# Performance work log

Measured on AMD Instinct MI355X. Metric: run time of the kernel, lower is better.

Reference implementation:

```python
import jax, jax.numpy as jnp
import numpy as np

N_NODES = 100000


def _add_self_loops(edge_index, n):
    loop = jnp.arange(n, dtype=edge_index.dtype)
    src = jnp.concatenate([edge_index[0], loop])
    dst = jnp.concatenate([edge_index[1], loop])
    return src, dst


def _gcn_conv(x, W, b, src, dst, n):
    # h = X W, then symmetric-normalized scatter-add over edges (PyG GCNConv)
    h = x @ W
    ones = jnp.ones(src.shape[0], dtype=h.dtype)
    deg = jax.ops.segment_sum(ones, dst, num_segments=n)  # in-degree incl. self loops
    dinv = jnp.where(deg > 0, jax.lax.rsqrt(deg), 0.0)
    norm = dinv[src] * dinv[dst]                           # [E]
    msg = h[src] * norm[:, None]                           # gather + scale
    out = jax.ops.segment_sum(msg, dst, num_segments=n)    # scatter-add
    return out + b


def setup_inputs() -> dict:
    key = jax.random.key(0)
    k1, k2, k3, k4 = jax.random.split(key, 4)
    F, H, C = 128, 128, 16
    x = jax.random.normal(k1, (N_NODES, F), dtype=jnp.float32)
    edge_index = jax.random.randint(k2, (2, 1600000), 0, N_NODES, dtype=jnp.int64)
    W1 = jax.random.normal(k3, (F, H), dtype=jnp.float32) / np.sqrt(F)
    b1 = jnp.zeros((H,), dtype=jnp.float32)
    W2 = jax.random.normal(k4, (H, C), dtype=jnp.float32) / np.sqrt(H)
    b2 = jnp.zeros((C,), dtype=jnp.float32)
    return {"x": x, "edge_index": edge_index, "W1": W1, "b1": b1, "W2": W2, "b2": b2}


def reference(x, edge_index, W1, b1, W2, b2):
    n = x.shape[0]
    src, dst = _add_self_loops(edge_index, n)
    h = _gcn_conv(x, W1, b1, src, dst, n)
    h = jax.nn.relu(h)
    # dropout(p=0.1) treated as identity (deterministic eval-mode reference)
    logits = _gcn_conv(h, W2, b2, src, dst, n)
    return logits, jax.nn.log_softmax(logits, axis=1)
```

## Files before the change

### kernel.cpp

```cpp
#include <hip/hip_runtime.h>
#include <math.h>


#define ELLW 72
#define EPB 16384
#define BSH 9
#define MAXBK 200
#define BCAP 10240

typedef __attribute__((ext_vector_type(8))) short short8;
typedef __attribute__((ext_vector_type(4))) float f32x4;
typedef __attribute__((ext_vector_type(4))) int i32x4;
typedef __attribute__((ext_vector_type(4))) _Float16 f16x4;
typedef __attribute__((ext_vector_type(8))) _Float16 f16x8;

__device__ __forceinline__ float bf2f(unsigned short u) {
    return __uint_as_float(((unsigned int)u) << 16);
}
__device__ __forceinline__ unsigned short f2bf(float f) {
    unsigned int u = __float_as_uint(f);
    unsigned int r = (u + 0x7fffu + ((u >> 16) & 1u)) >> 16;
    return (unsigned short)r;
}

__global__ __launch_bounds__(256) void k_bin_gemm(
        const int* __restrict__ src, const int* __restrict__ dst, int E,
        int* __restrict__ gcursor, int* __restrict__ binned, int nbuck, int neb,
        const float* __restrict__ x, const float* __restrict__ W1,
        unsigned short* __restrict__ h, int n) {
    __shared__ unsigned short xs[64 * 136];
    __shared__ unsigned short wtl[128 * 136];
    const int t = threadIdx.x;
    if ((int)blockIdx.x < neb) {
        int* cnt = (int*)xs;
        const int blk = blockIdx.x;
        for (int i = t; i < nbuck; i += 256) cnt[i] = 0;
        __syncthreads();
        const int e0 = blk * EPB;
        const int e1 = min(e0 + EPB, E);
        for (int e = e0 + t; e < e1; e += 256)
            atomicAdd(&cnt[dst[e] >> BSH], 1);
        __syncthreads();
        if (t < nbuck) {
            int c = cnt[t];
            cnt[t] = c ? atomicAdd(&gcursor[t], c) : 0;
        }
        __syncthreads();
        for (int e = e0 + t; e < e1; e += 256) {
            int d = dst[e];
            int b = d >> BSH;
            int r = atomicAdd(&cnt[b], 1);
            if (r < BCAP)
                binned[(size_t)b * BCAP + r] = src[e] | ((d & ((1 << BSH) - 1)) << 17);
        }
        return;
    }
    const int row0 = ((int)blockIdx.x - neb) * 64;
    for (int i = t; i < 2048; i += 256) {
        int r = i >> 5, c4 = (i & 31) << 2;
        int gr = row0 + r;
        float4 v = make_float4(0.f, 0.f, 0.f, 0.f);
        if (gr < n) v = *(const float4*)(x + (size_t)gr * 128 + c4);
        ushort4 u;
        u.x = f2bf(v.x); u.y = f2bf(v.y); u.z = f2bf(v.z); u.w = f2bf(v.w);
        *(ushort4*)(xs + r * 136 + c4) = u;
    }
    for (int i = t; i < 16384; i += 256) {
        int k = i >> 7, nc = i & 127;
        wtl[nc * 136 + k] = f2bf(W1[i]);
    }
    __syncthreads();
    const int w = t >> 6;
    const int lane = t & 63;
    const int m = lane & 15, q = lane >> 4;
    f32x4 acc[8];
#pragma unroll
    for (int ns = 0; ns < 8; ++ns) acc[ns] = (f32x4){0.f, 0.f, 0.f, 0.f};
#pragma unroll
    for (int kt = 0; kt < 4; ++kt) {
        short8 a = *(const short8*)(xs + (w * 16 + m) * 136 + kt * 32 + q * 8);
#pragma unroll
        for (int ns = 0; ns < 8; ++ns) {
            short8 b = *(const short8*)(wtl + (ns * 16 + m) * 136 + kt * 32 + q * 8);
            acc[ns] = __builtin_amdgcn_mfma_f32_16x16x32_bf16(a, b, acc[ns], 0, 0, 0);
        }
    }
    __syncthreads();
    unsigned short* xsw = xs + (w * 16) * 136;
#pragma unroll
    for (int ns = 0; ns < 8; ++ns)
#pragma unroll
        for (int reg = 0; reg < 4; ++reg)
            xsw[(q * 4 + reg) * 136 + ns * 16 + m] = f2bf(acc[ns][reg]);
    __syncthreads();
#pragma unroll
    for (int it = 0; it < 8; ++it) {
        int rl = (lane >> 5) + it * 2;
        int off = (lane & 31) * 4;
        int gr = row0 + w * 16 + rl;
        if (gr < n)
            *(ushort4*)(h + (size_t)gr * 128 + off) = *(const ushort4*)(xsw + rl * 136 + off);
    }
}

__global__ __launch_bounds__(256) void k_ell(
        const int* __restrict__ binned, const int* __restrict__ gcursor,
        int* __restrict__ deg, float* __restrict__ dinv, int* __restrict__ col,
        unsigned short* __restrict__ h, _Float16* __restrict__ g, int n) {
    __shared__ int sorted[BCAP];
    __shared__ int ldeg[1 << BSH];
    __shared__ int off[1 << BSH];
    __shared__ int cur[1 << BSH];
    __shared__ int psum[256];
    const int t = threadIdx.x, b = blockIdx.x;
    const int node0 = b << BSH;
    const size_t st = (size_t)b * BCAP;
    int cv = gcursor[b];
    if (cv > BCAP) cv = BCAP;
    if (b == 0) {
        if (t < 128) h[(size_t)n * 128 + t] = 0;
        if (t < 16) g[(size_t)n * 16 + t] = (_Float16)0.f;
        if (t == 0) dinv[n] = 1.f;
    }
    for (int i = t; i < (1 << BSH); i += 256) { ldeg[i] = 0; cur[i] = 0; }
    __syncthreads();
    for (int i = t; i < cv; i += 256)
        atomicAdd(&ldeg[binned[st + i] >> 17], 1);
    __syncthreads();
    int c0 = min(ldeg[2 * t], ELLW);
    int c1 = min(ldeg[2 * t + 1], ELLW);
    psum[t] = c0 + c1;
    __syncthreads();
    for (int o = 1; o < 256; o <<= 1) {
        int v = 0;
        if (t >= o) v = psum[t - o];
        __syncthreads();
        psum[t] += v;
        __syncthreads();
    }
    int base = psum[t] - (c0 + c1);
    off[2 * t] = base;
    off[2 * t + 1] = base + c0;
    __syncthreads();
    for (int i = t; i < cv; i += 256) {
        int v = binned[st + i];
        int dl = v >> 17;
        int r = atomicAdd(&cur[dl], 1);
        if (r < ELLW) sorted[off[dl] + r] = v & 0x1FFFF;
    }
    __syncthreads();
    const int nn = min(1 << BSH, n - node0);
    const int totv = nn * (ELLW / 4);
    int* colb = col + (size_t)node0 * ELLW;
    for (int idx = t; idx < totv; idx += 256) {
        int i = idx / (ELLW / 4);
        int q = (idx - i * (ELLW / 4)) * 4;
        int dc = min(ldeg[i], ELLW);
        int o = off[i];
        i32x4 v;
#pragma unroll
        for (int j = 0; j < 4; ++j)
            v[j] = (q + j < dc) ? sorted[o + q + j] : n;
        *(i32x4*)(colb + (size_t)i * ELLW + q) = v;
    }
    for (int i = t; i < (1 << BSH); i += 256) {
        int node = node0 + i;
        if (node < n) {
            int dgv = ldeg[i];
            deg[node] = dgv;
            dinv[node] = rsqrtf((float)(min(dgv, ELLW) + 1));
        }
    }
}

__global__ __launch_bounds__(256, 2) void k_gather1f(
        const unsigned short* __restrict__ h, const int* __restrict__ deg,
        const float* __restrict__ dinv, const int* __restrict__ col,
        const float* __restrict__ b1, const float* __restrict__ W2,
        _Float16* __restrict__ g, int n) {
    const int t = threadIdx.x;
    const int lane = t & 15;
    const int d = blockIdx.x * 16 + (t >> 4);
    if (d >= n) return;
    int dg = deg[d];
    if (dg > ELLW) dg = ELLW;
    const float dd = dinv[d];
    const int kend = (dg + 7) & ~7;
    const int* ecol = col + (size_t)d * ELLW;

    float aA[8], aB[8];
    {
        short8 u = *(const short8*)(h + (size_t)d * 128 + lane * 8);
#pragma unroll
        for (int j = 0; j < 8; ++j) {
            aA[j] = dd * bf2f((unsigned short)u[j]);
            aB[j] = 0.f;
        }
    }
    for (int k = 0; k < kend; k += 8) {
        int4 c0 = *(const int4*)(ecol + k);
        int4 c1 = *(const int4*)(ecol + k + 4);
        float e0 = dinv[c0.x], e1 = dinv[c0.y], e2 = dinv[c0.z], e3 = dinv[c0.w];
        float e4 = dinv[c1.x], e5 = dinv[c1.y], e6 = dinv[c1.z], e7 = dinv[c1.w];
        short8 u0 = *(const short8*)(h + (size_t)c0.x * 128 + lane * 8);
        short8 u1 = *(const short8*)(h + (size_t)c0.y * 128 + lane * 8);
        short8 u2 = *(const short8*)(h + (size_t)c0.z * 128 + lane * 8);
        short8 u3 = *(const short8*)(h + (size_t)c0.w * 128 + lane * 8);
        short8 u4 = *(const short8*)(h + (size_t)c1.x * 128 + lane * 8);
        short8 u5 = *(const short8*)(h + (size_t)c1.y * 128 + lane * 8);
        short8 u6 = *(const short8*)(h + (size_t)c1.z * 128 + lane * 8);
        short8 u7 = *(const short8*)(h + (size_t)c1.w * 128 + lane * 8);
#pragma unroll
        for (int j = 0; j < 8; ++j) {
            aA[j] = fmaf(bf2f((unsigned short)u0[j]), e0, aA[j]);
            aB[j] = fmaf(bf2f((unsigned short)u1[j]), e1, aB[j]);
            aA[j] = fmaf(bf2f((unsigned short)u2[j]), e2, aA[j]);
            aB[j] = fmaf(bf2f((unsigned short)u3[j]), e3, aB[j]);
            aA[j] = fmaf(bf2f((unsigned short)u4[j]), e4, aA[j]);
            aB[j] = fmaf(bf2f((unsigned short)u5[j]), e5, aB[j]);
            aA[j] = fmaf(bf2f((unsigned short)u6[j]), e6, aA[j]);
            aB[j] = fmaf(bf2f((unsigned short)u7[j]), e7, aB[j]);
        }
    }
    float y[8];
    const float* b1p = b1 + lane * 8;
#pragma unroll
    for (int j = 0; j < 8; ++j)
        y[j] = fmaxf(fmaf(aA[j] + aB[j], dd, b1p[j]), 0.f);
    const float4* w2v = (const float4*)(W2 + lane * 8 * 16);
    float4 z0 = make_float4(0.f, 0.f, 0.f, 0.f);
    float4 z1 = z0, z2 = z0, z3 = z0;
#pragma unroll
    for (int j = 0; j < 8; ++j) {
        float4 w0 = w2v[j * 4 + 0], w1 = w2v[j * 4 + 1];
        float4 w2 = w2v[j * 4 + 2], w3 = w2v[j * 4 + 3];
        float yj = y[j];
        z0.x = fmaf(yj, w0.x, z0.x); z0.y = fmaf(yj, w0.y, z0.y);
        z0.z = fmaf(yj, w0.z, z0.z); z0.w = fmaf(yj, w0.w, z0.w);
        z1.x = fmaf(yj, w1.x, z1.x); z1.y = fmaf(yj, w1.y, z1.y);
        z1.z = fmaf(yj, w1.z, z1.z); z1.w = fmaf(yj, w1.w, z1.w);
        z2.x = fmaf(yj, w2.x, z2.x); z2.y = fmaf(yj, w2.y, z2.y);
        z2.z = fmaf(yj, w2.z, z2.z); z2.w = fmaf(yj, w2.w, z2.w);
        z3.x = fmaf(yj, w3.x, z3.x); z3.y = fmaf(yj, w3.y, z3.y);
        z3.z = fmaf(yj, w3.z, z3.z); z3.w = fmaf(yj, w3.w, z3.w);
    }
#pragma unroll
    for (int mm = 1; mm < 16; mm <<= 1) {
        z0.x += __shfl_xor(z0.x, mm); z0.y += __shfl_xor(z0.y, mm);
        z0.z += __shfl_xor(z0.z, mm); z0.w += __shfl_xor(z0.w, mm);
        z1.x += __shfl_xor(z1.x, mm); z1.y += __shfl_xor(z1.y, mm);
        z1.z += __shfl_xor(z1.z, mm); z1.w += __shfl_xor(z1.w, mm);
        z2.x += __shfl_xor(z2.x, mm); z2.y += __shfl_xor(z2.y, mm);
        z2.z += __shfl_xor(z2.z, mm); z2.w += __shfl_xor(z2.w, mm);
        z3.x += __shfl_xor(z3.x, mm); z3.y += __shfl_xor(z3.y, mm);
        z3.z += __shfl_xor(z3.z, mm); z3.w += __shfl_xor(z3.w, mm);
    }
    if (lane < 4) {
        float4 z = (lane == 0) ? z0 : (lane == 1) ? z1 : (lane == 2) ? z2 : z3;
        f16x4 zz;
        zz[0] = (_Float16)(z.x * dd); zz[1] = (_Float16)(z.y * dd);
        zz[2] = (_Float16)(z.z * dd); zz[3] = (_Float16)(z.w * dd);
        *(f16x4*)(g + (size_t)d * 16 + lane * 4) = zz;
    }
}

__global__ void k_gather2(const _Float16* __restrict__ g, const int* __restrict__ deg,
                          const int* __restrict__ col, const float* __restrict__ b2,
                          float* __restrict__ out, int n) {
    const int t = threadIdx.x;
    const int d = blockIdx.x * 128 + (t >> 1);
    if (d >= n) return;
    const int l = t & 1;
    int dg = deg[d];
    if (dg > ELLW) dg = ELLW;
    const float dd = rsqrtf((float)(dg + 1));
    const int kend = (dg + 7) & ~7;
    const int* ecol = col + (size_t)d * ELLW;
    const _Float16* gl = g + l * 8;

    float aA[8], aB[8];
    {
        f16x8 s = *(const f16x8*)(gl + (size_t)d * 16);
#pragma unroll
        for (int j = 0; j < 8; ++j) { aA[j] = (float)s[j]; aB[j] = 0.f; }
    }
    for (int k = 0; k < kend; k += 8) {
        int4 c0 = *(const int4*)(ecol + k);
        int4 c1 = *(const int4*)(ecol + k + 4);
        f16x8 u0 = *(const f16x8*)(gl + (size_t)c0.x * 16);
        f16x8 u1 = *(const f16x8*)(gl + (size_t)c0.y * 16);
        f16x8 u2 = *(const f16x8*)(gl + (size_t)c0.z * 16);
        f16x8 u3 = *(const f16x8*)(gl + (size_t)c0.w * 16);
        f16x8 u4 = *(const f16x8*)(gl + (size_t)c1.x * 16);
        f16x8 u5 = *(const f16x8*)(gl + (size_t)c1.y * 16);
        f16x8 u6 = *(const f16x8*)(gl + (size_t)c1.z * 16);
        f16x8 u7 = *(const f16x8*)(gl + (size_t)c1.w * 16);
#pragma unroll
        for (int j = 0; j < 8; ++j) {
            aA[j] += (float)u0[j] + (float)u2[j] + (float)u4[j] + (float)u6[j];
            aB[j] += (float)u1[j] + (float)u3[j] + (float)u5[j] + (float)u7[j];
        }
    }
    float acc[8];
    const float* b2p = b2 + l * 8;
#pragma unroll
    for (int j = 0; j < 8; ++j) acc[j] = fmaf(aA[j] + aB[j], dd, b2p[j]);
    f32x4 o0 = {acc[0], acc[1], acc[2], acc[3]};
    f32x4 o1 = {acc[4], acc[5], acc[6], acc[7]};
    *(f32x4*)(out + (size_t)d * 16 + l * 8) = o0;
    *(f32x4*)(out + (size_t)d * 16 + l * 8 + 4) = o1;
    float m = acc[0];
#pragma unroll
    for (int j = 1; j < 8; ++j) m = fmaxf(m, acc[j]);
    m = fmaxf(m, __shfl_xor(m, 1));
    float e = 0.f;
#pragma unroll
    for (int j = 0; j < 8; ++j) e += expf(acc[j] - m);
    e += __shfl_xor(e, 1);
    float ls = m + logf(e);
    f32x4 p0, p1;
#pragma unroll
    for (int j = 0; j < 4; ++j) { p0[j] = acc[j] - ls; p1[j] = acc[j + 4] - ls; }
    float* ob = out + (size_t)n * 16 + (size_t)d * 16 + l * 8;
    *(f32x4*)(ob) = p0;
    *(f32x4*)(ob + 4) = p1;
}

static inline size_t align256(size_t v) { return (v + 255) & ~(size_t)255; }

extern "C" void kernel_launch(void* const* d_in, const int* in_sizes, int n_in,
                              void* d_out, int out_size, void* d_ws, size_t ws_size,
                              hipStream_t stream) {
    const float* x  = (const float*)d_in[0];
    const int*   ei = (const int*)d_in[1];
    const float* W1 = (const float*)d_in[2];
    const float* b1 = (const float*)d_in[3];
    const float* W2 = (const float*)d_in[4];
    const float* b2 = (const float*)d_in[5];
    float* out = (float*)d_out;

    const int n = in_sizes[0] / 128;
    const int E = in_sizes[1] / 2;
    const int* src = ei;
    const int* dst = ei + E;
    const int NEB = (E + EPB - 1) / EPB;
    const int NBUCK = (n + (1 << BSH) - 1) >> BSH;

    char* base = (char*)d_ws;
    size_t off = 0;
    int* deg = (int*)(base + off); off = align256(off + (size_t)n * 4);
    float* dinv = (float*)(base + off); off = align256(off + ((size_t)n + 1) * 4);
    int* col = (int*)(base + off); off = align256(off + (size_t)n * ELLW * 4);
    unsigned short* h = (unsigned short*)(base + off); off = align256(off + ((size_t)n + 1) * 128 * 2);
    _Float16* g = (_Float16*)(base + off); off = align256(off + ((size_t)n + 1) * 16 * 2);
    int* gcursor = (int*)(base + off); off = align256(off + (size_t)MAXBK * 4);
    int* binned = (int*)(base + off); off = align256(off + (size_t)NBUCK * BCAP * 4);

    hipMemsetAsync(gcursor, 0, (size_t)MAXBK * 4, stream);
    k_bin_gemm<<<NEB + (n + 63) / 64, 256, 0, stream>>>(
        src, dst, E, gcursor, binned, NBUCK, NEB, x, W1, h, n);
    k_ell<<<NBUCK, 256, 0, stream>>>(binned, gcursor, deg, dinv, col, h, g, n);
    k_gather1f<<<(n + 15) / 16, 256, 0, stream>>>(h, deg, dinv, col, b1, W2, g, n);
    k_gather2<<<(n + 127) / 128, 256, 0, stream>>>(g, deg, col, b2, out, n);
}
```

Baseline: 332.6 us.

## Fuse four GCN kernels into one persistent cooperative kernel with grid syncs

New measurement: 523.9 us. 1.58x slower.

```diff
diff --git a/kernel.cpp b/kernel.cpp
--- a/kernel.cpp
+++ b/kernel.cpp
@@ -1,5 +1,8 @@
 #include <hip/hip_runtime.h>
+#include <hip/hip_cooperative_groups.h>
 #include <math.h>
+
+namespace cg = cooperative_groups;
 
 
 #define ELLW 72
@@ -23,307 +26,318 @@
     return (unsigned short)r;
 }
 
-__global__ __launch_bounds__(256) void k_bin_gemm(
+__global__ __launch_bounds__(256) void k_fused(
         const int* __restrict__ src, const int* __restrict__ dst, int E,
         int* __restrict__ gcursor, int* __restrict__ binned, int nbuck, int neb,
         const float* __restrict__ x, const float* __restrict__ W1,
-        unsigned short* __restrict__ h, int n) {
-    __shared__ unsigned short xs[64 * 136];
-    __shared__ unsigned short wtl[128 * 136];
+        unsigned short* __restrict__ wt, unsigned short* __restrict__ h, int n,
+        int* __restrict__ deg, float* __restrict__ dinv, int* __restrict__ col,
+        const float* __restrict__ b1, const float* __restrict__ W2,
+        _Float16* __restrict__ g, const float* __restrict__ b2,
+        float* __restrict__ out, int gtiles, int t1, int t2) {
+    cg::grid_group grid = cg::this_grid();
+    __shared__ int smem_i[12032];
     const int t = threadIdx.x;
-    if ((int)blockIdx.x < neb) {
-        int* cnt = (int*)xs;
-        const int blk = blockIdx.x;
-        for (int i = t; i < nbuck; i += 256) cnt[i] = 0;
-        __syncthreads();
-        const int e0 = blk * EPB;
-        const int e1 = min(e0 + EPB, E);
-        for (int e = e0 + t; e < e1; e += 256)
-            atomicAdd(&cnt[dst[e] >> BSH], 1);
-        __syncthreads();
-        if (t < nbuck) {
-            int c = cnt[t];
-            cnt[t] = c ? atomicAdd(&gcursor[t], c) : 0;
-        }
-        __syncthreads();
-        for (int e = e0 + t; e < e1; e += 256) {
-            int d = dst[e];
-            int b = d >> BSH;
-            int r = atomicAdd(&cnt[b], 1);
-            if (r < BCAP)
-                binned[(size_t)b * BCAP + r] = src[e] | ((d & ((1 << BSH) - 1)) << 17);
-        }
-        return;
-    }
-    const int row0 = ((int)blockIdx.x - neb) * 64;
-    for (int i = t; i < 2048; i += 256) {
-        int r = i >> 5, c4 = (i & 31) << 2;
-        int gr = row0 + r;
-        float4 v = make_float4(0.f, 0.f, 0.f, 0.f);
-        if (gr < n) v = *(const float4*)(x + (size_t)gr * 128 + c4);
-        ushort4 u;
-        u.x = f2bf(v.x); u.y = f2bf(v.y); u.z = f2bf(v.z); u.w = f2bf(v.w);
-        *(ushort4*)(xs + r * 136 + c4) = u;
-    }
-    for (int i = t; i < 16384; i += 256) {
-        int k = i >> 7, nc = i & 127;
-        wtl[nc * 136 + k] = f2bf(W1[i]);
-    }
-    __syncthreads();
-    const int w = t >> 6;
-    const int lane = t & 63;
-    const int m = lane & 15, q = lane >> 4;
-    f32x4 acc[8];
-#pragma unroll
-    for (int ns = 0; ns < 8; ++ns) acc[ns] = (f32x4){0.f, 0.f, 0.f, 0.f};
-#pragma unroll
-    for (int kt = 0; kt < 4; ++kt) {
-        short8 a = *(const short8*)(xs + (w * 16 + m) * 136 + kt * 32 + q * 8);
-#pragma unroll
-        for (int ns = 0; ns < 8; ++ns) {
-            short8 b = *(const short8*)(wtl + (ns * 16 + m) * 136 + kt * 32 + q * 8);
-            acc[ns] = __builtin_amdgcn_mfma_f32_16x16x32_bf16(a, b, acc[ns], 0, 0, 0);
-        }
-    }
-    __syncthreads();
-    unsigned short* xsw = xs + (w * 16) * 136;
-#pragma unroll
-    for (int ns = 0; ns < 8; ++ns)
-#pragma unroll
-        for (int reg = 0; reg < 4; ++reg)
-            xsw[(q * 4 + reg) * 136 + ns * 16 + m] = f2bf(acc[ns][reg]);
-    __syncthreads();
-#pragma unroll
-    for (int it = 0; it < 8; ++it) {
-        int rl = (lane >> 5) + it * 2;
-        int off = (lane & 31) * 4;
-        int gr = row0 + w * 16 + rl;
-        if (gr < n)
-            *(ushort4*)(h + (size_t)gr * 128 + off) = *(const ushort4*)(xsw + rl * 136 + off);
-    }
-}
-
-__global__ __launch_bounds__(256) void k_ell(
-        const int* __restrict__ binned, const int* __restrict__ gcursor,
-        int* __restrict__ deg, float* __restrict__ dinv, int* __restrict__ col,
-        unsigned short* __restrict__ h, _Float16* __restrict__ g, int n) {
-    __shared__ int sorted[BCAP];
-    __shared__ int ldeg[1 << BSH];
-    __shared__ int off[1 << BSH];
-    __shared__ int cur[1 << BSH];
-    __shared__ int psum[256];
-    const int t = threadIdx.x, b = blockIdx.x;
-    const int node0 = b << BSH;
-    const size_t st = (size_t)b * BCAP;
-    int cv = gcursor[b];
-    if (cv > BCAP) cv = BCAP;
-    if (b == 0) {
+    const int nb = gridDim.x;
+
+    for (int i = blockIdx.x * 256 + t; i < 16384 + MAXBK; i += nb * 256) {
+        if (i < 16384) {
+            int nc = i >> 7, k = i & 127;
+            wt[i] = f2bf(W1[k * 128 + nc]);
+        } else {
+            gcursor[i - 16384] = 0;
+        }
+    }
+    if (blockIdx.x == 0) {
         if (t < 128) h[(size_t)n * 128 + t] = 0;
         if (t < 16) g[(size_t)n * 16 + t] = (_Float16)0.f;
         if (t == 0) dinv[n] = 1.f;
     }
-    for (int i = t; i < (1 << BSH); i += 256) { ldeg[i] = 0; cur[i] = 0; }
-    __syncthreads();
-    for (int i = t; i < cv; i += 256)
-        atomicAdd(&ldeg[binned[st + i] >> 17], 1);
-    __syncthreads();
-    int c0 = min(ldeg[2 * t], ELLW);
-    int c1 = min(ldeg[2 * t + 1], ELLW);
-    psum[t] = c0 + c1;
-    __syncthreads();
-    for (int o = 1; o < 256; o <<= 1) {
-        int v = 0;
-        if (t >= o) v = psum[t - o];
+    grid.sync();
+
+    for (int tile = blockIdx.x; tile < neb + gtiles; tile += nb) {
         __syncthreads();
-        psum[t] += v;
-        __syncthreads();
-    }
-    int base = psum[t] - (c0 + c1);
-    off[2 * t] = base;
-    off[2 * t + 1] = base + c0;
-    __syncthreads();
-    for (int i = t; i < cv; i += 256) {
-        int v = binned[st + i];
-        int dl = v >> 17;
-        int r = atomicAdd(&cur[dl], 1);
-        if (r < ELLW) sorted[off[dl] + r] = v & 0x1FFFF;
-    }
-    __syncthreads();
-    const int nn = min(1 << BSH, n - node0);
-    const int totv = nn * (ELLW / 4);
-    int* colb = col + (size_t)node0 * ELLW;
-    for (int idx = t; idx < totv; idx += 256) {
-        int i = idx / (ELLW / 4);
-        int q = (idx - i * (ELLW / 4)) * 4;
-        int dc = min(ldeg[i], ELLW);
-        int o = off[i];
-        i32x4 v;
-#pragma unroll
-        for (int j = 0; j < 4; ++j)
-            v[j] = (q + j < dc) ? sorted[o + q + j] : n;
-        *(i32x4*)(colb + (size_t)i * ELLW + q) = v;
-    }
-    for (int i = t; i < (1 << BSH); i += 256) {
-        int node = node0 + i;
-        if (node < n) {
-            int dgv = ldeg[i];
-            deg[node] = dgv;
-            dinv[node] = rsqrtf((float)(min(dgv, ELLW) + 1));
-        }
-    }
-}
-
-__global__ __launch_bounds__(256, 2) void k_gather1f(
-        const unsigned short* __restrict__ h, const int* __restrict__ deg,
-        const float* __restrict__ dinv, const int* __restrict__ col,
-        const float* __restrict__ b1, const float* __restrict__ W2,
-        _Float16* __restrict__ g, int n) {
-    const int t = threadIdx.x;
-    const int lane = t & 15;
-    const int d = blockIdx.x * 16 + (t >> 4);
-    if (d >= n) return;
-    int dg = deg[d];
-    if (dg > ELLW) dg = ELLW;
-    const float dd = dinv[d];
-    const int kend = (dg + 7) & ~7;
-    const int* ecol = col + (size_t)d * ELLW;
-
-    float aA[8], aB[8];
+        if (tile < neb) {
+            int* cnt = smem_i;
+            for (int i = t; i < nbuck; i += 256) cnt[i] = 0;
+            __syncthreads();
+            const int e0 = tile * EPB;
+            const int e1 = min(e0 + EPB, E);
+            for (int e = e0 + t; e < e1; e += 256)
+                atomicAdd(&cnt[dst[e] >> BSH], 1);
+            __syncthreads();
+            if (t < nbuck) {
+                int c = cnt[t];
+                cnt[t] = c ? atomicAdd(&gcursor[t], c) : 0;
+            }
+            __syncthreads();
+            for (int e = e0 + t; e < e1; e += 256) {
+                int d = dst[e];
+                int b = d >> BSH;
+                int r = atomicAdd(&cnt[b], 1);
+                if (r < BCAP)
+                    binned[(size_t)b * BCAP + r] =
+                        src[e] | ((d & ((1 << BSH) - 1)) << 17);
+            }
+        } else {
+            unsigned short* xs = (unsigned short*)smem_i;
+            const int row0 = (tile - neb) * 64;
+            for (int i = t; i < 2048; i += 256) {
+                int r = i >> 5, c4 = (i & 31) << 2;
+                int gr = row0 + r;
+                float4 v = make_float4(0.f, 0.f, 0.f, 0.f);
+                if (gr < n) v = *(const float4*)(x + (size_t)gr * 128 + c4);
+                ushort4 u;
+                u.x = f2bf(v.x); u.y = f2bf(v.y); u.z = f2bf(v.z); u.w = f2bf(v.w);
+                *(ushort4*)(xs + r * 136 + c4) = u;
+            }
+            __syncthreads();
+            const int w = t >> 6;
+            const int lane = t & 63;
+            const int m = lane & 15, q = lane >> 4;
+            f32x4 acc[8];
+#pragma unroll
+            for (int ns = 0; ns < 8; ++ns) acc[ns] = (f32x4){0.f, 0.f, 0.f, 0.f};
+#pragma unroll
+            for (int kt = 0; kt < 4; ++kt) {
+                short8 a = *(const short8*)(xs + (w * 16 + m) * 136 + kt * 32 + q * 8);
+#pragma unroll
+                for (int ns = 0; ns < 8; ++ns) {
+                    short8 b = *(const short8*)((const short*)wt +
+                               (ns * 16 + m) * 128 + kt * 32 + q * 8);
+                    acc[ns] = __builtin_amdgcn_mfma_f32_16x16x32_bf16(a, b, acc[ns], 0, 0, 0);
+                }
+            }
+            unsigned short* xsw = xs + (w * 16) * 136;
+#pragma unroll
+            for (int ns = 0; ns < 8; ++ns)
+#pragma unroll
+                for (int reg = 0; reg < 4; ++reg)
+                    xsw[(q * 4 + reg) * 136 + ns * 16 + m] = f2bf(acc[ns][reg]);
+            __syncthreads();
+#pragma unroll
+            for (int it = 0; it < 8; ++it) {
+                int rl = (lane >> 5) + it * 2;
+                int offb = (lane & 31) * 4;
+                int gr = row0 + w * 16 + rl;
+                if (gr < n)
+                    *(ushort4*)(h + (size_t)gr * 128 + offb) =
+                        *(const ushort4*)(xsw + rl * 136 + offb);
+            }
+        }
+    }
+    grid.sync();
+
     {
-        short8 u = *(const short8*)(h + (size_t)d * 128 + lane * 8);
-#pragma unroll
-        for (int j = 0; j < 8; ++j) {
-            aA[j] = dd * bf2f((unsigned short)u[j]);
-            aB[j] = 0.f;
-        }
-    }
-    for (int k = 0; k < kend; k += 8) {
-        int4 c0 = *(const int4*)(ecol + k);
-        int4 c1 = *(const int4*)(ecol + k + 4);
-        float e0 = dinv[c0.x], e1 = dinv[c0.y], e2 = dinv[c0.z], e3 = dinv[c0.w];
-        float e4 = dinv[c1.x], e5 = dinv[c1.y], e6 = dinv[c1.z], e7 = dinv[c1.w];
-        short8 u0 = *(const short8*)(h + (size_t)c0.x * 128 + lane * 8);
-        short8 u1 = *(const short8*)(h + (size_t)c0.y * 128 + lane * 8);
-        short8 u2 = *(const short8*)(h + (size_t)c0.z * 128 + lane * 8);
-        short8 u3 = *(const short8*)(h + (size_t)c0.w * 128 + lane * 8);
-        short8 u4 = *(const short8*)(h + (size_t)c1.x * 128 + lane * 8);
-        short8 u5 = *(const short8*)(h + (size_t)c1.y * 128 + lane * 8);
-        short8 u6 = *(const short8*)(h + (size_t)c1.z * 128 + lane * 8);
-        short8 u7 = *(const short8*)(h + (size_t)c1.w * 128 + lane * 8);
-#pragma unroll
-        for (int j = 0; j < 8; ++j) {
-            aA[j] = fmaf(bf2f((unsigned short)u0[j]), e0, aA[j]);
-            aB[j] = fmaf(bf2f((unsigned short)u1[j]), e1, aB[j]);
-            aA[j] = fmaf(bf2f((unsigned short)u2[j]), e2, aA[j]);
-            aB[j] = fmaf(bf2f((unsigned short)u3[j]), e3, aB[j]);
-            aA[j] = fmaf(bf2f((unsigned short)u4[j]), e4, aA[j]);
-            aB[j] = fmaf(bf2f((unsigned short)u5[j]), e5, aB[j]);
-            aA[j] = fmaf(bf2f((unsigned short)u6[j]), e6, aA[j]);
-            aB[j] = fmaf(bf2f((unsigned short)u7[j]), e7, aB[j]);
-        }
-    }
-    float y[8];
-    const float* b1p = b1 + lane * 8;
-#pragma unroll
-    for (int j = 0; j < 8; ++j)
-        y[j] = fmaxf(fmaf(aA[j] + aB[j], dd, b1p[j]), 0.f);
-    const float4* w2v = (const float4*)(W2 + lane * 8 * 16);
-    float4 z0 = make_float4(0.f, 0.f, 0.f, 0.f);
-    float4 z1 = z0, z2 = z0, z3 = z0;
-#pragma unroll
-    for (int j = 0; j < 8; ++j) {
-        float4 w0 = w2v[j * 4 + 0], w1 = w2v[j * 4 + 1];
-        float4 w2 = w2v[j * 4 + 2], w3 = w2v[j * 4 + 3];
-        float yj = y[j];
-        z0.x = fmaf(yj, w0.x, z0.x); z0.y = fmaf(yj, w0.y, z0.y);
-        z0.z = fmaf(yj, w0.z, z0.z); z0.w = fmaf(yj, w0.w, z0.w);
-        z1.x = fmaf(yj, w1.x, z1.x); z1.y = fmaf(yj, w1.y, z1.y);
-        z1.z = fmaf(yj, w1.z, z1.z); z1.w = fmaf(yj, w1.w, z1.w);
-        z2.x = fmaf(yj, w2.x, z2.x); z2.y = fmaf(yj, w2.y, z2.y);
-        z2.z = fmaf(yj, w2.z, z2.z); z2.w = fmaf(yj, w2.w, z2.w);
-        z3.x = fmaf(yj, w3.x, z3.x); z3.y = fmaf(yj, w3.y, z3.y);
-        z3.z = fmaf(yj, w3.z, z3.z); z3.w = fmaf(yj, w3.w, z3.w);
-    }
-#pragma unroll
-    for (int mm = 1; mm < 16; mm <<= 1) {
-        z0.x += __shfl_xor(z0.x, mm); z0.y += __shfl_xor(z0.y, mm);
-        z0.z += __shfl_xor(z0.z, mm); z0.w += __shfl_xor(z0.w, mm);
-        z1.x += __shfl_xor(z1.x, mm); z1.y += __shfl_xor(z1.y, mm);
-        z1.z += __shfl_xor(z1.z, mm); z1.w += __shfl_xor(z1.w, mm);
-        z2.x += __shfl_xor(z2.x, mm); z2.y += __shfl_xor(z2.y, mm);
-        z2.z += __shfl_xor(z2.z, mm); z2.w += __shfl_xor(z2.w, mm);
-        z3.x += __shfl_xor(z3.x, mm); z3.y += __shfl_xor(z3.y, mm);
-        z3.z += __shfl_xor(z3.z, mm); z3.w += __shfl_xor(z3.w, mm);
-    }
-    if (lane < 4) {
-        float4 z = (lane == 0) ? z0 : (lane == 1) ? z1 : (lane == 2) ? z2 : z3;
-        f16x4 zz;
-        zz[0] = (_Float16)(z.x * dd); zz[1] = (_Float16)(z.y * dd);
-        zz[2] = (_Float16)(z.z * dd); zz[3] = (_Float16)(z.w * dd);
-        *(f16x4*)(g + (size_t)d * 16 + lane * 4) = zz;
-    }
-}
-
-__global__ void k_gather2(const _Float16* __restrict__ g, const int* __restrict__ deg,
-                          const int* __restrict__ col, const float* __restrict__ b2,
-                          float* __restrict__ out, int n) {
-    const int t = threadIdx.x;
-    const int d = blockIdx.x * 128 + (t >> 1);
-    if (d >= n) return;
-    const int l = t & 1;
-    int dg = deg[d];
-    if (dg > ELLW) dg = ELLW;
-    const float dd = rsqrtf((float)(dg + 1));
-    const int kend = (dg + 7) & ~7;
-    const int* ecol = col + (size_t)d * ELLW;
-    const _Float16* gl = g + l * 8;
-
-    float aA[8], aB[8];
-    {
-        f16x8 s = *(const f16x8*)(gl + (size_t)d * 16);
-#pragma unroll
-        for (int j = 0; j < 8; ++j) { aA[j] = (float)s[j]; aB[j] = 0.f; }
-    }
-    for (int k = 0; k < kend; k += 8) {
-        int4 c0 = *(const int4*)(ecol + k);
-        int4 c1 = *(const int4*)(ecol + k + 4);
-        f16x8 u0 = *(const f16x8*)(gl + (size_t)c0.x * 16);
-        f16x8 u1 = *(const f16x8*)(gl + (size_t)c0.y * 16);
-        f16x8 u2 = *(const f16x8*)(gl + (size_t)c0.z * 16);
-        f16x8 u3 = *(const f16x8*)(gl + (size_t)c0.w * 16);
-        f16x8 u4 = *(const f16x8*)(gl + (size_t)c1.x * 16);
-        f16x8 u5 = *(const f16x8*)(gl + (size_t)c1.y * 16);
-        f16x8 u6 = *(const f16x8*)(gl + (size_t)c1.z * 16);
-        f16x8 u7 = *(const f16x8*)(gl + (size_t)c1.w * 16);
-#pragma unroll
-        for (int j = 0; j < 8; ++j) {
-            aA[j] += (float)u0[j] + (float)u2[j] + (float)u4[j] + (float)u6[j];
-            aB[j] += (float)u1[j] + (float)u3[j] + (float)u5[j] + (float)u7[j];
-        }
-    }
-    float acc[8];
-    const float* b2p = b2 + l * 8;
-#pragma unroll
-    for (int j = 0; j < 8; ++j) acc[j] = fmaf(aA[j] + aB[j], dd, b2p[j]);
-    f32x4 o0 = {acc[0], acc[1], acc[2], acc[3]};
-    f32x4 o1 = {acc[4], acc[5], acc[6], acc[7]};
-    *(f32x4*)(out + (size_t)d * 16 + l * 8) = o0;
-    *(f32x4*)(out + (size_t)d * 16 + l * 8 + 4) = o1;
-    float m = acc[0];
-#pragma unroll
-    for (int j = 1; j < 8; ++j) m = fmaxf(m, acc[j]);
-    m = fmaxf(m, __shfl_xor(m, 1));
-    float e = 0.f;
-#pragma unroll
-    for (int j = 0; j < 8; ++j) e += expf(acc[j] - m);
-    e += __shfl_xor(e, 1);
-    float ls = m + logf(e);
-    f32x4 p0, p1;
-#pragma unroll
-    for (int j = 0; j < 4; ++j) { p0[j] = acc[j] - ls; p1[j] = acc[j + 4] - ls; }
-    float* ob = out + (size_t)n * 16 + (size_t)d * 16 + l * 8;
-    *(f32x4*)(ob) = p0;
-    *(f32x4*)(ob + 4) = p1;
+        int* sorted = smem_i;
+        int* ldeg   = smem_i + BCAP;
+        int* offv   = smem_i + BCAP + 512;
+        int* cur    = smem_i + BCAP + 1024;
+        int* psum   = smem_i + BCAP + 1536;
+        for (int b = blockIdx.x; b < nbuck; b += nb) {
+            __syncthreads();
+            const int node0 = b << BSH;
+            const size_t st = (size_t)b * BCAP;
+            int cv = gcursor[b];
+            if (cv > BCAP) cv = BCAP;
+            for (int i = t; i < (1 << BSH); i += 256) { ldeg[i] = 0; cur[i] = 0; }
+            __syncthreads();
+            for (int i = t; i < cv; i += 256)
+                atomicAdd(&ldeg[binned[st + i] >> 17], 1);
+            __syncthreads();
+            int c0 = min(ldeg[2 * t], ELLW);
+            int c1 = min(ldeg[2 * t + 1], ELLW);
+            psum[t] = c0 + c1;
+            __syncthreads();
+            for (int o = 1; o < 256; o <<= 1) {
+                int v = 0;
+                if (t >= o) v = psum[t - o];
+                __syncthreads();
+                psum[t] += v;
+                __syncthreads();
+            }
+            int base = psum[t] - (c0 + c1);
+            offv[2 * t] = base;
+            offv[2 * t + 1] = base + c0;
+            __syncthreads();
+            for (int i = t; i < cv; i += 256) {
+                int v = binned[st + i];
+                int dl = v >> 17;
+                int r = atomicAdd(&cur[dl], 1);
+                if (r < ELLW) sorted[offv[dl] + r] = v & 0x1FFFF;
+            }
+            __syncthreads();
+            const int nn = min(1 << BSH, n - node0);
+            const int totv = nn * (ELLW / 4);
+            int* colb = col + (size_t)node0 * ELLW;
+            for (int idx = t; idx < totv; idx += 256) {
+                int i = idx / (ELLW / 4);
+                int q = (idx - i * (ELLW / 4)) * 4;
+                int dc = min(ldeg[i], ELLW);
+                int o = offv[i];
+                i32x4 v;
+#pragma unroll
+                for (int j = 0; j < 4; ++j)
+                    v[j] = (q + j < dc) ? sorted[o + q + j] : n;
+                *(i32x4*)(colb + (size_t)i * ELLW + q) = v;
+            }
+            for (int i = t; i < (1 << BSH); i += 256) {
+                int node = node0 + i;
+                if (node < n) {
+                    int dgv = ldeg[i];
+                    deg[node] = dgv;
+                    dinv[node] = rsqrtf((float)(min(dgv, ELLW) + 1));
+                }
+            }
+        }
+    }
+    grid.sync();
+
+    for (int tile = blockIdx.x; tile < t1; tile += nb) {
+        const int lane = t & 15;
+        const int d = tile * 16 + (t >> 4);
+        if (d < n) {
+            int dg = deg[d];
+            if (dg > ELLW) dg = ELLW;
+            const float dd = dinv[d];
+            const int kend = (dg + 7) & ~7;
+            const int* ecol = col + (size_t)d * ELLW;
+            float aA[8], aB[8];
+            {
+                short8 u = *(const short8*)(h + (size_t)d * 128 + lane * 8);
+#pragma unroll
+                for (int j = 0; j < 8; ++j) {
+                    aA[j] = dd * bf2f((unsigned short)u[j]);
+                    aB[j] = 0.f;
+                }
+            }
+            for (int k = 0; k < kend; k += 8) {
+                int4 c0 = *(const int4*)(ecol + k);
+                int4 c1 = *(const int4*)(ecol + k + 4);
+                float e0 = dinv[c0.x], e1 = dinv[c0.y], e2 = dinv[c0.z], e3 = dinv[c0.w];
+                float e4 = dinv[c1.x], e5 = dinv[c1.y], e6 = dinv[c1.z], e7 = dinv[c1.w];
+                short8 u0 = *(const short8*)(h + (size_t)c0.x * 128 + lane * 8);
+                short8 u1 = *(const short8*)(h + (size_t)c0.y * 128 + lane * 8);
+                short8 u2 = *(const short8*)(h + (size_t)c0.z * 128 + lane * 8);
+                short8 u3 = *(const short8*)(h + (size_t)c0.w * 128 + lane * 8);
+                short8 u4 = *(const short8*)(h + (size_t)c1.x * 128 + lane * 8);
+                short8 u5 = *(const short8*)(h + (size_t)c1.y * 128 + lane * 8);
+                short8 u6 = *(const short8*)(h + (size_t)c1.z * 128 + lane * 8);
+                short8 u7 = *(const short8*)(h + (size_t)c1.w * 128 + lane * 8);
+#pragma unroll
+                for (int j = 0; j < 8; ++j) {
+                    aA[j] = fmaf(bf2f((unsigned short)u0[j]), e0, aA[j]);
+                    aB[j] = fmaf(bf2f((unsigned short)u1[j]), e1, aB[j]);
+                    aA[j] = fmaf(bf2f((unsigned short)u2[j]), e2, aA[j]);
+                    aB[j] = fmaf(bf2f((unsigned short)u3[j]), e3, aB[j]);
+                    aA[j] = fmaf(bf2f((unsigned short)u4[j]), e4, aA[j]);
+                    aB[j] = fmaf(bf2f((unsigned short)u5[j]), e5, aB[j]);
+                    aA[j] = fmaf(bf2f((unsigned short)u6[j]), e6, aA[j]);
+                    aB[j] = fmaf(bf2f((unsigned short)u7[j]), e7, aB[j]);
+                }
+            }
+            float y[8];
+            const float* b1p = b1 + lane * 8;
+#pragma unroll
+            for (int j = 0; j < 8; ++j)
+                y[j] = fmaxf(fmaf(aA[j] + aB[j], dd, b1p[j]), 0.f);
+            const float4* w2v = (const float4*)(W2 + lane * 8 * 16);
+            float4 z0 = make_float4(0.f, 0.f, 0.f, 0.f);
+            float4 z1 = z0, z2 = z0, z3 = z0;
+#pragma unroll
+            for (int j = 0; j < 8; ++j) {
+                float4 w0 = w2v[j * 4 + 0], w1 = w2v[j * 4 + 1];
+                float4 w2 = w2v[j * 4 + 2], w3 = w2v[j * 4 + 3];
+                float yj = y[j];
+                z0.x = fmaf(yj, w0.x, z0.x); z0.y = fmaf(yj, w0.y, z0.y);
+                z0.z = fmaf(yj, w0.z, z0.z); z0.w = fmaf(yj, w0.w, z0.w);
+                z1.x = fmaf(yj, w1.x, z1.x); z1.y = fmaf(yj, w1.y, z1.y);
+                z1.z = fmaf(yj, w1.z, z1.z); z1.w = fmaf(yj, w1.w, z1.w);
+                z2.x = fmaf(yj, w2.x, z2.x); z2.y = fmaf(yj, w2.y, z2.y);
+                z2.z = fmaf(yj, w2.z, z2.z); z2.w = fmaf(yj, w2.w, z2.w);
+                z3.x = fmaf(yj, w3.x, z3.x); z3.y = fmaf(yj, w3.y, z3.y);
+                z3.z = fmaf(yj, w3.z, z3.z); z3.w = fmaf(yj, w3.w, z3.w);
+            }
+#pragma unroll
+            for (int mm = 1; mm < 16; mm <<= 1) {
+                z0.x += __shfl_xor(z0.x, mm); z0.y += __shfl_xor(z0.y, mm);
+                z0.z += __shfl_xor(z0.z, mm); z0.w += __shfl_xor(z0.w, mm);
+                z1.x += __shfl_xor(z1.x, mm); z1.y += __shfl_xor(z1.y, mm);
+                z1.z += __shfl_xor(z1.z, mm); z1.w += __shfl_xor(z1.w, mm);
+                z2.x += __shfl_xor(z2.x, mm); z2.y += __shfl_xor(z2.y, mm);
+                z2.z += __shfl_xor(z2.z, mm); z2.w += __shfl_xor(z2.w, mm);
+                z3.x += __shfl_xor(z3.x, mm); z3.y += __shfl_xor(z3.y, mm);
+                z3.z += __shfl_xor(z3.z, mm); z3.w += __shfl_xor(z3.w, mm);
+            }
+            if (lane < 4) {
+                float4 z = (lane == 0) ? z0 : (lane == 1) ? z1 : (lane == 2) ? z2 : z3;
+                f16x4 zz;
+                zz[0] = (_Float16)(z.x * dd); zz[1] = (_Float16)(z.y * dd);
+                zz[2] = (_Float16)(z.z * dd); zz[3] = (_Float16)(z.w * dd);
+                *(f16x4*)(g + (size_t)d * 16 + lane * 4) = zz;
+            }
+        }
+    }
+    grid.sync();
+
+    for (int tile = blockIdx.x; tile < t2; tile += nb) {
+        const int d = tile * 128 + (t >> 1);
+        if (d < n) {
+            const int l = t & 1;
+            int dg = deg[d];
+            if (dg > ELLW) dg = ELLW;
+            const float dd = rsqrtf((float)(dg + 1));
+            const int kend = (dg + 7) & ~7;
+            const int* ecol = col + (size_t)d * ELLW;
+            const _Float16* gl = g + l * 8;
+            float aA[8], aB[8];
+            {
+                f16x8 s = *(const f16x8*)(gl + (size_t)d * 16);
+#pragma unroll
+                for (int j = 0; j < 8; ++j) { aA[j] = (float)s[j]; aB[j] = 0.f; }
+            }
+            for (int k = 0; k < kend; k += 8) {
+                int4 c0 = *(const int4*)(ecol + k);
+                int4 c1 = *(const int4*)(ecol + k + 4);
+                f16x8 u0 = *(const f16x8*)(gl + (size_t)c0.x * 16);
+                f16x8 u1 = *(const f16x8*)(gl + (size_t)c0.y * 16);
+                f16x8 u2 = *(const f16x8*)(gl + (size_t)c0.z * 16);
+                f16x8 u3 = *(const f16x8*)(gl + (size_t)c0.w * 16);
+                f16x8 u4 = *(const f16x8*)(gl + (size_t)c1.x * 16);
+                f16x8 u5 = *(const f16x8*)(gl + (size_t)c1.y * 16);
+                f16x8 u6 = *(const f16x8*)(gl + (size_t)c1.z * 16);
+                f16x8 u7 = *(const f16x8*)(gl + (size_t)c1.w * 16);
+#pragma unroll
+                for (int j = 0; j < 8; ++j) {
+                    aA[j] += (float)u0[j] + (float)u2[j] + (float)u4[j] + (float)u6[j];
+                    aB[j] += (float)u1[j] + (float)u3[j] + (float)u5[j] + (float)u7[j];
+                }
+            }
+            float acc[8];
+            const float* b2p = b2 + l * 8;
+#pragma unroll
+            for (int j = 0; j < 8; ++j) acc[j] = fmaf(aA[j] + aB[j], dd, b2p[j]);
+            f32x4 o0 = {acc[0], acc[1], acc[2], acc[3]};
+            f32x4 o1 = {acc[4], acc[5], acc[6], acc[7]};
+            *(f32x4*)(out + (size_t)d * 16 + l * 8) = o0;
+            *(f32x4*)(out + (size_t)d * 16 + l * 8 + 4) = o1;
+            float m = acc[0];
+#pragma unroll
+            for (int j = 1; j < 8; ++j) m = fmaxf(m, acc[j]);
+            m = fmaxf(m, __shfl_xor(m, 1));
+            float e = 0.f;
+#pragma unroll
+            for (int j = 0; j < 8; ++j) e += expf(acc[j] - m);
+            e += __shfl_xor(e, 1);
+            float ls = m + logf(e);
+            f32x4 p0, p1;
+#pragma unroll
+            for (int j = 0; j < 4; ++j) { p0[j] = acc[j] - ls; p1[j] = acc[j + 4] - ls; }
+            float* ob = out + (size_t)n * 16 + (size_t)d * 16 + l * 8;
+            *(f32x4*)(ob) = p0;
+            *(f32x4*)(ob + 4) = p1;
+        }
+    }
 }
 
 static inline size_t align256(size_t v) { return (v + 255) & ~(size_t)255; }
@@ -339,27 +353,44 @@
     const float* b2 = (const float*)d_in[5];
     float* out = (float*)d_out;
 
-    const int n = in_sizes[0] / 128;
-    const int E = in_sizes[1] / 2;
+    int n = in_sizes[0] / 128;
+    int E = in_sizes[1] / 2;
     const int* src = ei;
     const int* dst = ei + E;
-    const int NEB = (E + EPB - 1) / EPB;
-    const int NBUCK = (n + (1 << BSH) - 1) >> BSH;
+    int NEB = (E + EPB - 1) / EPB;
+    int NBUCK = (n + (1 << BSH) - 1) >> BSH;
 
     char* base = (char*)d_ws;
     size_t off = 0;
     int* deg = (int*)(base + off); off = align256(off + (size_t)n * 4);
     float* dinv = (float*)(base + off); off = align256(off + ((size_t)n + 1) * 4);
     int* col = (int*)(base + off); off = align256(off + (size_t)n * ELLW * 4);
+    unsigned short* wt = (unsigned short*)(base + off); off = align256(off + 128 * 128 * 2);
     unsigned short* h = (unsigned short*)(base + off); off = align256(off + ((size_t)n + 1) * 128 * 2);
     _Float16* g = (_Float16*)(base + off); off = align256(off + ((size_t)n + 1) * 16 * 2);
     int* gcursor = (int*)(base + off); off = align256(off + (size_t)MAXBK * 4);
     int* binned = (int*)(base + off); off = align256(off + (size_t)NBUCK * BCAP * 4);
 
-    hipMemsetAsync(gcursor, 0, (size_t)MAXBK * 4, stream);
-    k_bin_gemm<<<NEB + (n + 63) / 64, 256, 0, stream>>>(
-        src, dst, E, gcursor, binned, NBUCK, NEB, x, W1, h, n);
-    k_ell<<<NBUCK, 256, 0, stream>>>(binned, gcursor, deg, dinv, col, h, g, n);
-    k_gather1f<<<(n + 15) / 16, 256, 0, stream>>>(h, deg, dinv, col, b1, W2, g, n);
-    k_gather2<<<(n + 127) / 128, 256, 0, stream>>>(g, deg, col, b2, out, n);
+    static int s_grid = 0;
+    if (s_grid == 0) {
+        int dev = 0;
+        hipGetDevice(&dev);
+        hipDeviceProp_t prop;
+        hipGetDeviceProperties(&prop, dev);
+        int nbl = 0;
+        hipOccupancyMaxActiveBlocksPerMultiprocessor(&nbl, k_fused, 256, 0);
+        if (nbl < 1) nbl = 1;
+        s_grid = nbl * prop.multiProcessorCount;
+    }
+    int gtiles = (n + 63) / 64;
+    int t1 = (n + 15) / 16;
+    int t2 = (n + 127) / 128;
+
+    void* args[] = {
+        (void*)&src, (void*)&dst, (void*)&E, (void*)&gcursor, (void*)&binned,
+        (void*)&NBUCK, (void*)&NEB, (void*)&x, (void*)&W1, (void*)&wt,
+        (void*)&h, (void*)&n, (void*)&deg, (void*)&dinv, (void*)&col,
+        (void*)&b1, (void*)&W2, (void*)&g, (void*)&b2, (void*)&out,
+        (void*)&gtiles, (void*)&t1, (void*)&t2};
+    hipLaunchCooperativeKernel(k_fused, dim3(s_grid), dim3(256), args, 0u, stream);
 }
```
